# Kernel optimization log

Hardware: AMD Instinct MI355X
Metric: run time of the kernel (lower is better)

## Reference

```python
import jax, jax.numpy as jnp
import numpy as np
import math

SEGMENT_LENGTHS = [2048, 4096, 8192]
DILATION_RATES = [1, 2, 4]


def setup_inputs() -> dict:
    key = jax.random.key(0)
    kq, kk, kv = jax.random.split(key, 3)
    b, n, h, d = 2, 8192, 32, 128
    q = jax.random.normal(kq, (b, n, h, d), dtype=jnp.float32)
    k = jax.random.normal(kk, (b, n, h, d), dtype=jnp.float32)
    v = jax.random.normal(kv, (b, n, h, d), dtype=jnp.float32)
    return {"q": q, "k": k, "v": v}


def _dilated_attention(q, k, v):
    # Faithful translation of _compute_dilated_attention.
    # NOTE: torch.matmul on (b, S, h, d) with transpose(-2, -1) contracts over
    # head_dim d and yields (b, S, h, h) scores: heads attend to heads at a
    # single (possibly dilated) key position. We reproduce that exactly.
    b, n, h, d = q.shape
    scale = 1.0 / math.sqrt(d)
    out = jnp.zeros_like(q)
    for seg_len, dil in zip(SEGMENT_LENGTHS, DILATION_RATES):
        if seg_len > n:
            continue
        n_seg = n // seg_len
        cov = n_seg * seg_len
        # (b, n_seg, seg_len, h, d)
        qs = q[:, :cov].reshape(b, n_seg, seg_len, h, d)
        if dil == 1:
            ks = k[:, :cov].reshape(b, n_seg, seg_len, h, d)
            vs = v[:, :cov].reshape(b, n_seg, seg_len, h, d)
        else:
            # idx[g, i] = g*seg_len + i*dil, clamped to n-1 (matches the loop)
            idx = (jnp.arange(n_seg)[:, None] * seg_len
                   + jnp.arange(seg_len)[None, :] * dil)
            idx = jnp.minimum(idx, n - 1)  # (n_seg, seg_len)
            ks = k[:, idx]  # (b, n_seg, seg_len, h, d)
            vs = v[:, idx]
        scores = jnp.einsum('bgsid,bgsjd->bgsij', qs, ks) * scale  # (b,g,s,h,h)
        attn = jax.nn.softmax(scores, axis=-1)
        res = jnp.einsum('bgsij,bgsjd->bgsid', attn, vs)
        # later configs overwrite earlier ones, as in the torch loop
        out = out.at[:, :cov].set(res.reshape(b, cov, h, d))
    return out


def reference(q, k, v):
    # world_size == 1 -> hierarchy level 1 -> _local_forward with all heads
    # local, which is just _compute_dilated_attention.
    return _dilated_attention(q, k, v)
```

## Files before the change

### kernel.cpp

```cpp
#include <hip/hip_runtime.h>
#include <hip/hip_bf16.h>

typedef __attribute__((ext_vector_type(4))) float f32x4;
typedef __attribute__((ext_vector_type(8))) __bf16 bf16x8;

#define NCTX 8192
#define DH 128
#define ROWE 4096
#define SC2 0.12751705766482797f
#define KSTR 136
#define PSTR 40
#define OSTR 132
#define BUFS (32*KSTR)
#define NPRIV 1024
#define NSHRD 768
#define ITERS 8

__device__ __forceinline__ unsigned f2bf(float x) {
  union { float f; unsigned u; } un; un.f = x;
  return (un.u + 0x7FFFu + ((un.u >> 16) & 1u)) >> 16;
}
__device__ __forceinline__ unsigned pk2(float a, float b) {
  float2 t; t.x = a; t.y = b;
  union { __hip_bfloat162 h; unsigned u; } un;
  un.h = __float22bfloat162_rn(t);
  return un.u;
}

template<bool NT>
__device__ __forceinline__ void stage_row(const float* __restrict__ src,
                                          unsigned short* dst, int lane) {
  const int jb = lane >> 5, d = 4 * (lane & 31);
#pragma unroll
  for (int half = 0; half < 2; ++half) {
    f32x4 x[8];
#pragma unroll
    for (int ch = 0; ch < 8; ++ch) {
      const f32x4* p = reinterpret_cast<const f32x4*>(src + 4*lane + 256*(half*8 + ch));
      x[ch] = NT ? __builtin_nontemporal_load(p) : *p;
    }
#pragma unroll
    for (int ch = 0; ch < 8; ++ch) {
      const int j = jb + 2*(half*8 + ch);
      uint2 wv;
      wv.x = pk2(x[ch][0], x[ch][1]);
      wv.y = pk2(x[ch][2], x[ch][3]);
      *reinterpret_cast<uint2*>(&dst[j*KSTR + d]) = wv;
    }
  }
}

__device__ __forceinline__ void gather_va(const unsigned short* vbuf,
                                          bf16x8* va, int c, int g) {
#pragma unroll
  for (int dt = 0; dt < 8; ++dt) {
    unsigned t0 = vbuf[(g*8 + 0)*KSTR + dt*16 + c];
    unsigned t1 = vbuf[(g*8 + 1)*KSTR + dt*16 + c];
    unsigned t2 = vbuf[(g*8 + 2)*KSTR + dt*16 + c];
    unsigned t3 = vbuf[(g*8 + 3)*KSTR + dt*16 + c];
    unsigned t4 = vbuf[(g*8 + 4)*KSTR + dt*16 + c];
    unsigned t5 = vbuf[(g*8 + 5)*KSTR + dt*16 + c];
    unsigned t6 = vbuf[(g*8 + 6)*KSTR + dt*16 + c];
    unsigned t7 = vbuf[(g*8 + 7)*KSTR + dt*16 + c];
    union { unsigned u[4]; bf16x8 f; } un;
    un.u[0] = t0 | (t1 << 16); un.u[1] = t2 | (t3 << 16);
    un.u[2] = t4 | (t5 << 16); un.u[3] = t6 | (t7 << 16);
    va[dt] = un.f;
  }
}

__global__ __launch_bounds__(256, 3) void hda(
    const float* __restrict__ q, const float* __restrict__ kg,
    const float* __restrict__ v, float* __restrict__ out)
{
  extern __shared__ __align__(16) unsigned short lds[];

  const int tid  = threadIdx.x;
  const int w    = tid >> 6;
  const int lane = tid & 63;
  const int c = lane & 15;
  const int g = lane >> 4;
  const int jb = lane >> 5, dcol = 4 * (lane & 31);

  unsigned short* sb = lds + w * BUFS;

  if (blockIdx.x < NPRIV) {
    const int p = blockIdx.x * 4 + w;
    const int b = p >> 11;
    const int s = p & 2047;
    const int r = 4 * s;

    const float* qsrc = q  + ((size_t)b * NCTX + s) * ROWE;
    const float* ksrc = kg + ((size_t)b * NCTX + r) * ROWE;
    const float* vsrc = v  + ((size_t)b * NCTX + r) * ROWE;
    float*       op   = out + ((size_t)b * NCTX + s) * ROWE;

    stage_row<true>(qsrc, sb, lane);
    bf16x8 qa[2][4];
#pragma unroll
    for (int t = 0; t < 2; ++t)
#pragma unroll
      for (int ks = 0; ks < 4; ++ks)
        qa[t][ks] = *reinterpret_cast<const bf16x8*>(&sb[(t*16 + c)*KSTR + ks*32 + g*8]);

    stage_row<false>(ksrc, sb, lane);
    bf16x8 kf[2][4];
#pragma unroll
    for (int t = 0; t < 2; ++t)
#pragma unroll
      for (int ks = 0; ks < 4; ++ks)
        kf[t][ks] = *reinterpret_cast<const bf16x8*>(&sb[(t*16 + c)*KSTR + ks*32 + g*8]);

    f32x4 vx[8];
#pragma unroll
    for (int ch = 0; ch < 8; ++ch)
      vx[ch] = *reinterpret_cast<const f32x4*>(vsrc + 4*lane + 256*ch);
    __builtin_amdgcn_sched_barrier(0);

    f32x4 S[2][2];
#pragma unroll
    for (int it = 0; it < 2; ++it)
#pragma unroll
      for (int jt = 0; jt < 2; ++jt) {
        f32x4 acc = (f32x4)0.0f;
#pragma unroll
        for (int ks = 0; ks < 4; ++ks)
          acc = __builtin_amdgcn_mfma_f32_16x16x32_bf16(qa[it][ks], kf[jt][ks], acc, 0, 0, 0);
        S[it][jt] = acc;
      }

#pragma unroll
    for (int ch = 0; ch < 8; ++ch) {
      uint2 wv;
      wv.x = pk2(vx[ch][0], vx[ch][1]);
      wv.y = pk2(vx[ch][2], vx[ch][3]);
      *reinterpret_cast<uint2*>(&sb[(jb + 2*ch)*KSTR + dcol]) = wv;
    }
#pragma unroll
    for (int ch = 0; ch < 8; ++ch)
      vx[ch] = *reinterpret_cast<const f32x4*>(vsrc + 4*lane + 256*(8 + ch));
    __builtin_amdgcn_sched_barrier(0);

    float pp[2][2][4], inv[2][4];
#pragma unroll
    for (int it = 0; it < 2; ++it) {
      float ls[4] = {0.f, 0.f, 0.f, 0.f};
#pragma unroll
      for (int jt = 0; jt < 2; ++jt)
#pragma unroll
        for (int rr = 0; rr < 4; ++rr) {
          float e = exp2f(S[it][jt][rr] * SC2);
          pp[it][jt][rr] = e;
          ls[rr] += e;
        }
#pragma unroll
      for (int m = 1; m <= 8; m <<= 1)
#pragma unroll
        for (int rr = 0; rr < 4; ++rr)
          ls[rr] += __shfl_xor(ls[rr], m);
#pragma unroll
      for (int rr = 0; rr < 4; ++rr) inv[it][rr] = 1.0f / ls[rr];
    }

#pragma unroll
    for (int ch = 0; ch < 8; ++ch) {
      uint2 wv;
      wv.x = pk2(vx[ch][0], vx[ch][1]);
      wv.y = pk2(vx[ch][2], vx[ch][3]);
      *reinterpret_cast<uint2*>(&sb[(jb + 2*(8 + ch))*KSTR + dcol]) = wv;
    }

    bf16x8 va[8];
    gather_va(sb, va, c, g);

#pragma unroll
    for (int it = 0; it < 2; ++it)
#pragma unroll
      for (int jt = 0; jt < 2; ++jt)
#pragma unroll
        for (int rr = 0; rr < 4; ++rr)
          sb[(it*16 + g*4 + rr)*PSTR + jt*16 + c] =
              (unsigned short)f2bf(pp[it][jt][rr] * inv[it][rr]);

    bf16x8 pa[2];
    pa[0] = *reinterpret_cast<const bf16x8*>(&sb[c*PSTR + g*8]);
    pa[1] = *reinterpret_cast<const bf16x8*>(&sb[(16 + c)*PSTR + g*8]);

    float* ob = reinterpret_cast<float*>(sb);
#pragma unroll
    for (int it = 0; it < 2; ++it) {
      f32x4 o[8];
#pragma unroll
      for (int dt = 0; dt < 8; ++dt)
        o[dt] = __builtin_amdgcn_mfma_f32_16x16x32_bf16(va[dt], pa[it], (f32x4)0.0f, 0, 0, 0);
#pragma unroll
      for (int dt = 0; dt < 8; ++dt)
        *reinterpret_cast<f32x4*>(&ob[c*OSTR + dt*16 + g*4]) = o[dt];
#pragma unroll
      for (int ch = 0; ch < 8; ++ch) {
        const int flat = 4*lane + 256*ch;
        const int row = flat >> 7, col = flat & 127;
        f32x4 y = *reinterpret_cast<const f32x4*>(&ob[row*OSTR + col]);
        __builtin_nontemporal_store(y, reinterpret_cast<f32x4*>(op + it*2048 + flat));
      }
    }
    return;
  }

  const int gw = (blockIdx.x - NPRIV) * 4 + w;
  const int b  = (gw >= 1536) ? 1 : 0;
  const size_t frbase = (size_t)(gw - b*1536) * 128;
  const float* qbase = q   + ((size_t)b*262144 + 65536 + frbase) * DH;
  float*       obase = out + ((size_t)b*262144 + 65536 + frbase) * DH;
  const float* k8 = kg + ((size_t)b * NCTX + (NCTX-1)) * ROWE;
  const float* v8 = v  + ((size_t)b * NCTX + (NCTX-1)) * ROWE;

  stage_row<false>(k8, sb, lane);
  bf16x8 kf[2][4];
#pragma unroll
  for (int t = 0; t < 2; ++t)
#pragma unroll
    for (int ks = 0; ks < 4; ++ks)
      kf[t][ks] = *reinterpret_cast<const bf16x8*>(&sb[(t*16 + c)*KSTR + ks*32 + g*8]);

  stage_row<false>(v8, sb, lane);
  bf16x8 va[8];
  gather_va(sb, va, c, g);

  {
    f32x4 x[8];
#pragma unroll
    for (int ch = 0; ch < 8; ++ch)
      x[ch] = __builtin_nontemporal_load(
          reinterpret_cast<const f32x4*>(qbase + 4*lane + 256*ch));
#pragma unroll
    for (int ch = 0; ch < 8; ++ch) {
      uint2 wv;
      wv.x = pk2(x[ch][0], x[ch][1]);
      wv.y = pk2(x[ch][2], x[ch][3]);
      *reinterpret_cast<uint2*>(&sb[(jb + 2*ch)*KSTR + dcol]) = wv;
    }
  }

  f32x4 pf[8];
#pragma unroll 1
  for (int iter = 0; iter < ITERS; ++iter) {
    bf16x8 qa[4];
#pragma unroll
    for (int ks = 0; ks < 4; ++ks)
      qa[ks] = *reinterpret_cast<const bf16x8*>(&sb[c*KSTR + ks*32 + g*8]);

    if (iter + 1 < ITERS) {
#pragma unroll
      for (int ch = 0; ch < 8; ++ch)
        pf[ch] = __builtin_nontemporal_load(reinterpret_cast<const f32x4*>(
            qbase + (size_t)(iter + 1) * 2048 + 4*lane + 256*ch));
      __builtin_amdgcn_sched_barrier(0);
    }

    f32x4 S[2];
#pragma unroll
    for (int jt = 0; jt < 2; ++jt) {
      f32x4 acc = (f32x4)0.0f;
#pragma unroll
      for (int ks = 0; ks < 4; ++ks)
        acc = __builtin_amdgcn_mfma_f32_16x16x32_bf16(qa[ks], kf[jt][ks], acc, 0, 0, 0);
      S[jt] = acc;
    }

    float pp[2][4], ls[4] = {0.f, 0.f, 0.f, 0.f};
#pragma unroll
    for (int jt = 0; jt < 2; ++jt)
#pragma unroll
      for (int rr = 0; rr < 4; ++rr) {
        float e = exp2f(S[jt][rr] * SC2);
        pp[jt][rr] = e;
        ls[rr] += e;
      }
#pragma unroll
    for (int m = 1; m <= 8; m <<= 1)
#pragma unroll
      for (int rr = 0; rr < 4; ++rr)
        ls[rr] += __shfl_xor(ls[rr], m);
    float inv[4];
#pragma unroll
    for (int rr = 0; rr < 4; ++rr) inv[rr] = 1.0f / ls[rr];

#pragma unroll
    for (int jt = 0; jt < 2; ++jt)
#pragma unroll
      for (int rr = 0; rr < 4; ++rr)
        sb[(g*4 + rr)*PSTR + jt*16 + c] =
            (unsigned short)f2bf(pp[jt][rr] * inv[rr]);
    bf16x8 pa = *reinterpret_cast<const bf16x8*>(&sb[c*PSTR + g*8]);

    f32x4 o[8];
#pragma unroll
    for (int dt = 0; dt < 8; ++dt)
      o[dt] = __builtin_amdgcn_mfma_f32_16x16x32_bf16(va[dt], pa, (f32x4)0.0f, 0, 0, 0);
    float* ob = reinterpret_cast<float*>(sb);
#pragma unroll
    for (int dt = 0; dt < 8; ++dt)
      *reinterpret_cast<f32x4*>(&ob[c*OSTR + dt*16 + g*4]) = o[dt];
#pragma unroll
    for (int ch = 0; ch < 8; ++ch) {
      const int flat = 4*lane + 256*ch;
      const int row = flat >> 7, col = flat & 127;
      f32x4 y = *reinterpret_cast<const f32x4*>(&ob[row*OSTR + col]);
      __builtin_nontemporal_store(y, reinterpret_cast<f32x4*>(
          obase + (size_t)iter * 2048 + flat));
    }

    if (iter + 1 < ITERS) {
#pragma unroll
      for (int ch = 0; ch < 8; ++ch) {
        uint2 wv;
        wv.x = pk2(pf[ch][0], pf[ch][1]);
        wv.y = pk2(pf[ch][2], pf[ch][3]);
        *reinterpret_cast<uint2*>(&sb[(jb + 2*ch)*KSTR + dcol]) = wv;
      }
    }
  }
}

extern "C" void kernel_launch(void* const* d_in, const int* in_sizes, int n_in,
                              void* d_out, int out_size, void* d_ws, size_t ws_size,
                              hipStream_t stream) {
  const float* q = (const float*)d_in[0];
  const float* k = (const float*)d_in[1];
  const float* v = (const float*)d_in[2];
  float* o = (float*)d_out;
  hda<<<dim3(NPRIV + NSHRD, 1, 1), dim3(256, 1, 1), 4 * BUFS * 2, stream>>>(q, k, v, o);
}
```

Before: 118.1 us.

## Share clamped K/V row per block and split shared-query work across more blocks

For the shared-row region, where every dilated key index is clamped to row n-1, the block now stages the K and V row in LDS once for all four waves behind a block barrier, instead of each wave staging them privately. Each wave handles two positions per iteration (32 head rows) instead of eight 16-row chunks. The shared-region grid doubles so more blocks carry less serial work each. This cuts redundant K/V loads and conversions but adds LDS per block and a __syncthreads, which may lower occupancy.

```diff
diff --git a/kernel.cpp b/kernel.cpp
--- a/kernel.cpp
+++ b/kernel.cpp
@@ -13,8 +13,7 @@
 #define OSTR 132
 #define BUFS (32*KSTR)
 #define NPRIV 1024
-#define NSHRD 768
-#define ITERS 8
+#define NSHRD 1536
 
 __device__ __forceinline__ unsigned f2bf(float x) {
   union { float f; unsigned u; } un; un.f = x;
@@ -50,25 +49,6 @@
   }
 }
 
-__device__ __forceinline__ void gather_va(const unsigned short* vbuf,
-                                          bf16x8* va, int c, int g) {
-#pragma unroll
-  for (int dt = 0; dt < 8; ++dt) {
-    unsigned t0 = vbuf[(g*8 + 0)*KSTR + dt*16 + c];
-    unsigned t1 = vbuf[(g*8 + 1)*KSTR + dt*16 + c];
-    unsigned t2 = vbuf[(g*8 + 2)*KSTR + dt*16 + c];
-    unsigned t3 = vbuf[(g*8 + 3)*KSTR + dt*16 + c];
-    unsigned t4 = vbuf[(g*8 + 4)*KSTR + dt*16 + c];
-    unsigned t5 = vbuf[(g*8 + 5)*KSTR + dt*16 + c];
-    unsigned t6 = vbuf[(g*8 + 6)*KSTR + dt*16 + c];
-    unsigned t7 = vbuf[(g*8 + 7)*KSTR + dt*16 + c];
-    union { unsigned u[4]; bf16x8 f; } un;
-    un.u[0] = t0 | (t1 << 16); un.u[1] = t2 | (t3 << 16);
-    un.u[2] = t4 | (t5 << 16); un.u[3] = t6 | (t7 << 16);
-    va[dt] = un.f;
-  }
-}
-
 __global__ __launch_bounds__(256, 3) void hda(
     const float* __restrict__ q, const float* __restrict__ kg,
     const float* __restrict__ v, float* __restrict__ out)
@@ -171,7 +151,21 @@
     }
 
     bf16x8 va[8];
-    gather_va(sb, va, c, g);
+#pragma unroll
+    for (int dt = 0; dt < 8; ++dt) {
+      unsigned t0 = sb[(g*8 + 0)*KSTR + dt*16 + c];
+      unsigned t1 = sb[(g*8 + 1)*KSTR + dt*16 + c];
+      unsigned t2 = sb[(g*8 + 2)*KSTR + dt*16 + c];
+      unsigned t3 = sb[(g*8 + 3)*KSTR + dt*16 + c];
+      unsigned t4 = sb[(g*8 + 4)*KSTR + dt*16 + c];
+      unsigned t5 = sb[(g*8 + 5)*KSTR + dt*16 + c];
+      unsigned t6 = sb[(g*8 + 6)*KSTR + dt*16 + c];
+      unsigned t7 = sb[(g*8 + 7)*KSTR + dt*16 + c];
+      union { unsigned u[4]; bf16x8 f; } un;
+      un.u[0] = t0 | (t1 << 16); un.u[1] = t2 | (t3 << 16);
+      un.u[2] = t4 | (t5 << 16); un.u[3] = t6 | (t7 << 16);
+      va[dt] = un.f;
+    }
 
 #pragma unroll
     for (int it = 0; it < 2; ++it)
@@ -207,117 +201,150 @@
     return;
   }
 
-  const int gw = (blockIdx.x - NPRIV) * 4 + w;
-  const int b  = (gw >= 1536) ? 1 : 0;
-  const size_t frbase = (size_t)(gw - b*1536) * 128;
-  const float* qbase = q   + ((size_t)b*262144 + 65536 + frbase) * DH;
-  float*       obase = out + ((size_t)b*262144 + 65536 + frbase) * DH;
-  const float* k8 = kg + ((size_t)b * NCTX + (NCTX-1)) * ROWE;
-  const float* v8 = v  + ((size_t)b * NCTX + (NCTX-1)) * ROWE;
-
-  stage_row<false>(k8, sb, lane);
-  bf16x8 kf[2][4];
-#pragma unroll
-  for (int t = 0; t < 2; ++t)
-#pragma unroll
-    for (int ks = 0; ks < 4; ++ks)
-      kf[t][ks] = *reinterpret_cast<const bf16x8*>(&sb[(t*16 + c)*KSTR + ks*32 + g*8]);
-
-  stage_row<false>(v8, sb, lane);
-  bf16x8 va[8];
-  gather_va(sb, va, c, g);
+  const int bi = blockIdx.x - NPRIV;
+  const int b  = (bi >= 768) ? 1 : 0;
+  const int sA = 2048 + (bi - b*768)*8 + w*2;
+
+  const float* qb_ = q   + (size_t)b * NCTX * ROWE;
+  float*       ob_ = out + (size_t)b * NCTX * ROWE;
+  const unsigned short* kbuf = lds + 4*BUFS;
+  const unsigned short* vbuf = lds + 5*BUFS;
 
   {
-    f32x4 x[8];
-#pragma unroll
-    for (int ch = 0; ch < 8; ++ch)
-      x[ch] = __builtin_nontemporal_load(
-          reinterpret_cast<const f32x4*>(qbase + 4*lane + 256*ch));
-#pragma unroll
-    for (int ch = 0; ch < 8; ++ch) {
-      uint2 wv;
-      wv.x = pk2(x[ch][0], x[ch][1]);
-      wv.y = pk2(x[ch][2], x[ch][3]);
-      *reinterpret_cast<uint2*>(&sb[(jb + 2*ch)*KSTR + dcol]) = wv;
-    }
+    const float* kr8 = kg + ((size_t)b * NCTX + (NCTX-1)) * ROWE;
+    const float* vr8 = v  + ((size_t)b * NCTX + (NCTX-1)) * ROWE;
+    const int d0 = 4 * (tid & 31), jj = tid >> 5;
+#pragma unroll
+    for (int ch = 0; ch < 4; ++ch) {
+      const int fo = 4*tid + 1024*ch;
+      const int j  = jj + 8*ch;
+      f32x4 xk = *reinterpret_cast<const f32x4*>(kr8 + fo);
+      f32x4 xv = *reinterpret_cast<const f32x4*>(vr8 + fo);
+      uint2 wk, wv2;
+      wk.x  = pk2(xk[0], xk[1]); wk.y  = pk2(xk[2], xk[3]);
+      wv2.x = pk2(xv[0], xv[1]); wv2.y = pk2(xv[2], xv[3]);
+      *reinterpret_cast<uint2*>(&lds[4*BUFS + j*KSTR + d0]) = wk;
+      *reinterpret_cast<uint2*>(&lds[5*BUFS + j*KSTR + d0]) = wv2;
+    }
+    __syncthreads();
   }
 
-  f32x4 pf[8];
+  stage_row<true>(qb_ + (size_t)sA * ROWE, sb, lane);
+  f32x4 q1[16];
+#pragma unroll
+  for (int ch = 0; ch < 16; ++ch)
+    q1[ch] = __builtin_nontemporal_load(reinterpret_cast<const f32x4*>(
+        qb_ + (size_t)(sA + 1) * ROWE + 4*lane + 256*ch));
+  __builtin_amdgcn_sched_barrier(0);
+
 #pragma unroll 1
-  for (int iter = 0; iter < ITERS; ++iter) {
-    bf16x8 qa[4];
-#pragma unroll
-    for (int ks = 0; ks < 4; ++ks)
-      qa[ks] = *reinterpret_cast<const bf16x8*>(&sb[c*KSTR + ks*32 + g*8]);
-
-    if (iter + 1 < ITERS) {
-#pragma unroll
-      for (int ch = 0; ch < 8; ++ch)
-        pf[ch] = __builtin_nontemporal_load(reinterpret_cast<const f32x4*>(
-            qbase + (size_t)(iter + 1) * 2048 + 4*lane + 256*ch));
-      __builtin_amdgcn_sched_barrier(0);
-    }
-
-    f32x4 S[2];
-#pragma unroll
-    for (int jt = 0; jt < 2; ++jt) {
-      f32x4 acc = (f32x4)0.0f;
+  for (int i = 0; i < 2; ++i) {
+    const int s = sA + i;
+
+    if (i == 1) {
+#pragma unroll
+      for (int ch = 0; ch < 16; ++ch) {
+        uint2 wv;
+        wv.x = pk2(q1[ch][0], q1[ch][1]);
+        wv.y = pk2(q1[ch][2], q1[ch][3]);
+        *reinterpret_cast<uint2*>(&sb[(jb + 2*ch)*KSTR + dcol]) = wv;
+      }
+    }
+
+    bf16x8 qa[2][4];
+#pragma unroll
+    for (int t = 0; t < 2; ++t)
 #pragma unroll
       for (int ks = 0; ks < 4; ++ks)
-        acc = __builtin_amdgcn_mfma_f32_16x16x32_bf16(qa[ks], kf[jt][ks], acc, 0, 0, 0);
-      S[jt] = acc;
-    }
-
-    float pp[2][4], ls[4] = {0.f, 0.f, 0.f, 0.f};
-#pragma unroll
-    for (int jt = 0; jt < 2; ++jt)
-#pragma unroll
-      for (int rr = 0; rr < 4; ++rr) {
-        float e = exp2f(S[jt][rr] * SC2);
-        pp[jt][rr] = e;
-        ls[rr] += e;
-      }
-#pragma unroll
-    for (int m = 1; m <= 8; m <<= 1)
-#pragma unroll
-      for (int rr = 0; rr < 4; ++rr)
-        ls[rr] += __shfl_xor(ls[rr], m);
-    float inv[4];
-#pragma unroll
-    for (int rr = 0; rr < 4; ++rr) inv[rr] = 1.0f / ls[rr];
-
-#pragma unroll
-    for (int jt = 0; jt < 2; ++jt)
-#pragma unroll
-      for (int rr = 0; rr < 4; ++rr)
-        sb[(g*4 + rr)*PSTR + jt*16 + c] =
-            (unsigned short)f2bf(pp[jt][rr] * inv[rr]);
-    bf16x8 pa = *reinterpret_cast<const bf16x8*>(&sb[c*PSTR + g*8]);
-
-    f32x4 o[8];
-#pragma unroll
-    for (int dt = 0; dt < 8; ++dt)
-      o[dt] = __builtin_amdgcn_mfma_f32_16x16x32_bf16(va[dt], pa, (f32x4)0.0f, 0, 0, 0);
+        qa[t][ks] = *reinterpret_cast<const bf16x8*>(&sb[(t*16 + c)*KSTR + ks*32 + g*8]);
+
+    bf16x8 kf[2][4];
+#pragma unroll
+    for (int t = 0; t < 2; ++t)
+#pragma unroll
+      for (int ks = 0; ks < 4; ++ks)
+        kf[t][ks] = *reinterpret_cast<const bf16x8*>(&kbuf[(t*16 + c)*KSTR + ks*32 + g*8]);
+
+    f32x4 S[2][2];
+#pragma unroll
+    for (int it = 0; it < 2; ++it)
+#pragma unroll
+      for (int jt = 0; jt < 2; ++jt) {
+        f32x4 acc = (f32x4)0.0f;
+#pragma unroll
+        for (int ks = 0; ks < 4; ++ks)
+          acc = __builtin_amdgcn_mfma_f32_16x16x32_bf16(qa[it][ks], kf[jt][ks], acc, 0, 0, 0);
+        S[it][jt] = acc;
+      }
+
+    float pp[2][2][4], inv[2][4];
+#pragma unroll
+    for (int it = 0; it < 2; ++it) {
+      float ls[4] = {0.f, 0.f, 0.f, 0.f};
+#pragma unroll
+      for (int jt = 0; jt < 2; ++jt)
+#pragma unroll
+        for (int rr = 0; rr < 4; ++rr) {
+          float e = exp2f(S[it][jt][rr] * SC2);
+          pp[it][jt][rr] = e;
+          ls[rr] += e;
+        }
+#pragma unroll
+      for (int m = 1; m <= 8; m <<= 1)
+#pragma unroll
+        for (int rr = 0; rr < 4; ++rr)
+          ls[rr] += __shfl_xor(ls[rr], m);
+#pragma unroll
+      for (int rr = 0; rr < 4; ++rr) inv[it][rr] = 1.0f / ls[rr];
+    }
+
+    bf16x8 va[8];
+#pragma unroll
+    for (int dt = 0; dt < 8; ++dt) {
+      unsigned t0 = vbuf[(g*8 + 0)*KSTR + dt*16 + c];
+      unsigned t1 = vbuf[(g*8 + 1)*KSTR + dt*16 + c];
+      unsigned t2 = vbuf[(g*8 + 2)*KSTR + dt*16 + c];
+      unsigned t3 = vbuf[(g*8 + 3)*KSTR + dt*16 + c];
+      unsigned t4 = vbuf[(g*8 + 4)*KSTR + dt*16 + c];
+      unsigned t5 = vbuf[(g*8 + 5)*KSTR + dt*16 + c];
+      unsigned t6 = vbuf[(g*8 + 6)*KSTR + dt*16 + c];
+      unsigned t7 = vbuf[(g*8 + 7)*KSTR + dt*16 + c];
+      union { unsigned u[4]; bf16x8 f; } un;
+      un.u[0] = t0 | (t1 << 16); un.u[1] = t2 | (t3 << 16);
+      un.u[2] = t4 | (t5 << 16); un.u[3] = t6 | (t7 << 16);
+      va[dt] = un.f;
+    }
+
+#pragma unroll
+    for (int it = 0; it < 2; ++it)
+#pragma unroll
+      for (int jt = 0; jt < 2; ++jt)
+#pragma unroll
+        for (int rr = 0; rr < 4; ++rr)
+          sb[(it*16 + g*4 + rr)*PSTR + jt*16 + c] =
+              (unsigned short)f2bf(pp[it][jt][rr] * inv[it][rr]);
+
+    bf16x8 pa[2];
+    pa[0] = *reinterpret_cast<const bf16x8*>(&sb[c*PSTR + g*8]);
+    pa[1] = *reinterpret_cast<const bf16x8*>(&sb[(16 + c)*PSTR + g*8]);
+
+    float* op = ob_ + (size_t)s * ROWE;
     float* ob = reinterpret_cast<float*>(sb);
 #pragma unroll
-    for (int dt = 0; dt < 8; ++dt)
-      *reinterpret_cast<f32x4*>(&ob[c*OSTR + dt*16 + g*4]) = o[dt];
-#pragma unroll
-    for (int ch = 0; ch < 8; ++ch) {
-      const int flat = 4*lane + 256*ch;
-      const int row = flat >> 7, col = flat & 127;
-      f32x4 y = *reinterpret_cast<const f32x4*>(&ob[row*OSTR + col]);
-      __builtin_nontemporal_store(y, reinterpret_cast<f32x4*>(
-          obase + (size_t)iter * 2048 + flat));
-    }
-
-    if (iter + 1 < ITERS) {
+    for (int it = 0; it < 2; ++it) {
+      f32x4 o[8];
+#pragma unroll
+      for (int dt = 0; dt < 8; ++dt)
+        o[dt] = __builtin_amdgcn_mfma_f32_16x16x32_bf16(va[dt], pa[it], (f32x4)0.0f, 0, 0, 0);
+#pragma unroll
+      for (int dt = 0; dt < 8; ++dt)
+        *reinterpret_cast<f32x4*>(&ob[c*OSTR + dt*16 + g*4]) = o[dt];
 #pragma unroll
       for (int ch = 0; ch < 8; ++ch) {
-        uint2 wv;
-        wv.x = pk2(pf[ch][0], pf[ch][1]);
-        wv.y = pk2(pf[ch][2], pf[ch][3]);
-        *reinterpret_cast<uint2*>(&sb[(jb + 2*ch)*KSTR + dcol]) = wv;
+        const int flat = 4*lane + 256*ch;
+        const int row = flat >> 7, col = flat & 127;
+        f32x4 y = *reinterpret_cast<const f32x4*>(&ob[row*OSTR + col]);
+        __builtin_nontemporal_store(y, reinterpret_cast<f32x4*>(op + it*2048 + flat));
       }
     }
   }
@@ -330,5 +357,5 @@
   const float* k = (const float*)d_in[1];
   const float* v = (const float*)d_in[2];
   float* o = (float*)d_out;
-  hda<<<dim3(NPRIV + NSHRD, 1, 1), dim3(256, 1, 1), 4 * BUFS * 2, stream>>>(q, k, v, o);
-}
+  hda<<<dim3(NPRIV + NSHRD, 1, 1), dim3(256, 1, 1), 6 * BUFS * 2, stream>>>(q, k, v, o);
+}
```

After: 115.6 us. -2.1%, faster.
